# Kernel tuning notes

Measured on AMD Instinct MI355X. Metric: run time of the kernel, lower is better.

The kernel has to match this reference:

```python
import jax, jax.numpy as jnp
import numpy as np
import math

C, D, N = 10000, 128, 16384

def setup_inputs() -> dict:
    key = jax.random.key(0)
    kz, kmu = jax.random.split(key)
    z = jax.random.normal(kz, (N, D), dtype=jnp.float32)
    mu = jax.random.normal(kmu, (C, D), dtype=jnp.float32) * (6.0 / math.sqrt(2 * D))
    log_cov = jnp.zeros((1,), dtype=jnp.float32)
    prior_logits = jnp.zeros((C,), dtype=jnp.float32)
    return {"z": z, "mu": mu, "log_cov": log_cov, "prior_logits": prior_logits}

def reference(z, mu, log_cov, prior_logits):
    # m2[n,c] = ||z_n - mu_c||^2 = ||z_n||^2 - 2 z_n.mu_c + ||mu_c||^2 (GEMM form,
    # algebraically identical to the explicit broadcast-diff in the torch source)
    z_sq = jnp.sum(z * z, axis=-1, keepdims=True)          # [N,1]
    mu_sq = jnp.sum(mu * mu, axis=-1)                      # [C]
    cross = jnp.einsum('nd,cd->nc', z, mu)                 # [N,C] GEMM
    m2 = z_sq - 2.0 * cross + mu_sq[None, :]               # [N,C]
    lc = log_cov[0]
    var = jnp.exp(lc)
    log_det = D * lc
    log_prior = jax.nn.log_softmax(prior_logits, axis=0)   # [C]
    return log_prior[None, :] - 0.5 * (m2 / var + log_det)
```

## Files before the change

### kernel.cpp

```cpp
#include <hip/hip_runtime.h>

#define N_DIM 16384
#define C_DIM 10000
#define D_DIM 128
#define CT 79
#define C_PAD 10240
#define BM 64
#define BN 128
#define MT 256
#define ZPB 2048
#define MPB 1280

typedef __attribute__((ext_vector_type(8))) short bf16x8;
typedef __attribute__((ext_vector_type(4))) float f32x4;
typedef __attribute__((ext_vector_type(2))) unsigned int uint2v;

static __device__ __forceinline__ unsigned short f2bf(float x) {
  unsigned int u = __float_as_uint(x);
  u += 0x7fffu + ((u >> 16) & 1u);
  return (unsigned short)(u >> 16);
}

__global__ __launch_bounds__(256) void prep_kernel(
    const float* __restrict__ z, const float* __restrict__ mu,
    const float* __restrict__ log_cov, const float* __restrict__ prior,
    unsigned short* __restrict__ zb, unsigned short* __restrict__ mub,
    float* __restrict__ atbl, float* __restrict__ btbl, float* __restrict__ lse_out) {
  const int bid = blockIdx.x;
  const int tid = threadIdx.x;
  if (bid < ZPB + MPB) {
    const bool isz = bid < ZPB;
    const int lane = tid & 63;
    const int row = (isz ? bid : bid - ZPB) * 8 + ((tid >> 6) << 1) + (lane >> 5);
    const int col = (lane & 31) * 4;
    const int nrows = isz ? N_DIM : C_DIM;
    f32x4 v = {0.f, 0.f, 0.f, 0.f};
    if (row < nrows)
      v = *(const f32x4*)((isz ? z : mu) + (size_t)row * D_DIM + col);
    float ss = v[0]*v[0] + v[1]*v[1] + v[2]*v[2] + v[3]*v[3];
    #pragma unroll
    for (int off = 16; off; off >>= 1) ss += __shfl_down(ss, off, 32);
    float lc = log_cov[0];
    float iv = expf(-lc);
    if (isz) { v[0]*=iv; v[1]*=iv; v[2]*=iv; v[3]*=iv; }
    uint2v packed;
    packed[0] = (unsigned int)f2bf(v[0]) | ((unsigned int)f2bf(v[1]) << 16);
    packed[1] = (unsigned int)f2bf(v[2]) | ((unsigned int)f2bf(v[3]) << 16);
    int cb = (lane & 31) * 8;
    if (isz) {
      *(uint2v*)((char*)zb + (size_t)row * 256 + cb) = packed;
    } else {
      *(uint2v*)((char*)mub + (size_t)row * 256 + (cb ^ ((row & 7) << 4))) = packed;
    }
    if ((lane & 31) == 0) {
      if (isz) {
        atbl[row] = -0.5f * ss * iv;
      } else {
        btbl[row] = (row < C_DIM)
            ? (prior[row] - 0.5f * ss * iv - 0.5f * (float)D_DIM * lc) : 0.f;
      }
    }
  } else {
    __shared__ float red[256];
    const f32x4* p4 = (const f32x4*)prior;
    float m = -1e30f;
    for (int i = tid; i < C_DIM / 4; i += 256) {
      f32x4 v = p4[i];
      m = fmaxf(fmaxf(fmaxf(m, v[0]), fmaxf(v[1], v[2])), v[3]);
    }
    red[tid] = m; __syncthreads();
    for (int s = 128; s; s >>= 1) {
      if (tid < s) red[tid] = fmaxf(red[tid], red[tid + s]);
      __syncthreads();
    }
    float mx = red[0]; __syncthreads();
    float sum = 0.f;
    for (int i = tid; i < C_DIM / 4; i += 256) {
      f32x4 v = p4[i];
      sum += expf(v[0] - mx) + expf(v[1] - mx) + expf(v[2] - mx) + expf(v[3] - mx);
    }
    red[tid] = sum; __syncthreads();
    for (int s = 128; s; s >>= 1) {
      if (tid < s) red[tid] += red[tid + s];
      __syncthreads();
    }
    if (tid == 0) *lse_out = mx + logf(red[0]);
  }
}

__global__ __launch_bounds__(256, 4) void lda_main_kernel(
    const unsigned short* __restrict__ zb, const unsigned short* __restrict__ mub,
    const float* __restrict__ atbl, const float* __restrict__ btbl,
    const float* __restrict__ lse_p, const float* __restrict__ log_cov,
    float* __restrict__ out) {
  __shared__ char lds[BN * 256];

  const int ct = blockIdx.x;
  const int mt = blockIdx.y;
  const int tid = threadIdx.x;
  const int rbase = mt * BM;
  const int cbase = ct * BN;
  const int wid = tid >> 6;
  const int lane = tid & 63;
  const int l15 = lane & 15;
  const int lq = lane >> 4;

  {
    const char* gm = (const char*)mub + (size_t)cbase * 256 + wid * 8192 + lane * 16;
    char* lm = lds + wid * 8192;
    #pragma unroll
    for (int it = 0; it < 8; ++it)
      __builtin_amdgcn_global_load_lds(
          (const __attribute__((address_space(1))) void*)(gm + it * 1024),
          (__attribute__((address_space(3))) void*)(lm + it * 1024), 16, 0, 0);
  }

  const int zrow = rbase + wid * 16 + l15;
  bf16x8 zf[4];
  #pragma unroll
  for (int kk = 0; kk < 4; ++kk)
    zf[kk] = *(const bf16x8*)((const char*)zb + (size_t)zrow * 256 + kk * 64 + lq * 16);

  const int l31 = lane & 31;
  const float lse = lse_p[0];
  f32x4 btv = *(const f32x4*)&btbl[cbase + l31 * 4];
  btv[0] -= lse; btv[1] -= lse; btv[2] -= lse; btv[3] -= lse;

  __syncthreads();

  f32x4 acc[8] = {};
  #pragma unroll
  for (int kk = 0; kk < 4; ++kk) {
    const int kbyte = kk * 64 + lq * 16;
    bf16x8 mf[8];
    #pragma unroll
    for (int a = 0; a < 8; ++a) {
      int row = a * 16 + l15;
      mf[a] = *(const bf16x8*)(lds + row * 256 + (kbyte ^ ((row & 7) << 4)));
    }
    #pragma unroll
    for (int a = 0; a < 8; ++a)
      acc[a] = __builtin_amdgcn_mfma_f32_16x16x32_bf16(mf[a], zf[kk], acc[a], 0, 0, 0);
  }

  __syncthreads();

  const int mloc = wid * 16 + l15;
  #pragma unroll
  for (int a = 0; a < 8; ++a) {
    int cb4 = (a * 16 + lq * 4) * 4;
    *(f32x4*)(lds + mloc * 512 + (cb4 ^ ((mloc & 7) << 4))) = acc[a];
  }

  const int hl = lane >> 5;
  #pragma unroll
  for (int i = 0; i < 16; i += 2) {
    int m = wid * 16 + i + hl;
    int rowg = rbase + m;
    f32x4 t = *(const f32x4*)(lds + m * 512 + ((l31 * 16) ^ ((m & 7) << 4)));
    float av = atbl[rowg];
    int cg = cbase + l31 * 4;
    if (cg < C_DIM) {
      f32x4 v;
      #pragma unroll
      for (int r = 0; r < 4; ++r) v[r] = av + btv[r] + t[r];
      __builtin_nontemporal_store(v, (f32x4*)(out + (size_t)rowg * C_DIM + cg));
    }
  }
}

extern "C" void kernel_launch(void* const* d_in, const int* in_sizes, int n_in,
                              void* d_out, int out_size, void* d_ws, size_t ws_size,
                              hipStream_t stream) {
  const float* z     = (const float*)d_in[0];
  const float* mu    = (const float*)d_in[1];
  const float* lcov  = (const float*)d_in[2];
  const float* prior = (const float*)d_in[3];
  float* out = (float*)d_out;

  char* w = (char*)d_ws;
  unsigned short* zb  = (unsigned short*)w;
  unsigned short* mub = (unsigned short*)(w + 4194304);
  float* atbl = (float*)(w + 4194304 + 2621440);
  float* btbl = atbl + N_DIM;
  float* lse  = btbl + C_PAD;

  prep_kernel<<<ZPB + MPB + 1, 256, 0, stream>>>(z, mu, lcov, prior,
                                                 zb, mub, atbl, btbl, lse);
  dim3 grid(CT, MT);
  lda_main_kernel<<<grid, 256, 0, stream>>>(zb, mub, atbl, btbl, lse, lcov, out);
}
```

Baseline: 128.4 us.

## Load GEMM fragments directly from global per wave and drop shared mu staging

The main kernel no longer stages the mu tile into LDS with global_load_lds and no longer needs a block barrier before the MFMA loop. Each wave now owns a 32-column strip and reads mu and z fragments straight from global memory into registers, computing a 32x64 sub-tile. The epilogue transposes through a per-wave LDS region without barriers, and the prep kernel stops swizzling mu. Global and L2 traffic goes up because z fragments are re-read by all four waves, in exchange for removing the synchronization and the LDS loads.

After: 255.2 us. 1.99x slower.

```diff
diff --git a/kernel.cpp b/kernel.cpp
--- a/kernel.cpp
+++ b/kernel.cpp
@@ -47,11 +47,7 @@
     packed[0] = (unsigned int)f2bf(v[0]) | ((unsigned int)f2bf(v[1]) << 16);
     packed[1] = (unsigned int)f2bf(v[2]) | ((unsigned int)f2bf(v[3]) << 16);
     int cb = (lane & 31) * 8;
-    if (isz) {
-      *(uint2v*)((char*)zb + (size_t)row * 256 + cb) = packed;
-    } else {
-      *(uint2v*)((char*)mub + (size_t)row * 256 + (cb ^ ((row & 7) << 4))) = packed;
-    }
+    *(uint2v*)((char*)(isz ? zb : mub) + (size_t)row * 256 + cb) = packed;
     if ((lane & 31) == 0) {
       if (isz) {
         atbl[row] = -0.5f * ss * iv;
@@ -93,73 +89,62 @@
     const float* __restrict__ atbl, const float* __restrict__ btbl,
     const float* __restrict__ lse_p, const float* __restrict__ log_cov,
     float* __restrict__ out) {
-  __shared__ char lds[BN * 256];
+  __shared__ char lds[4 * 8192];
 
   const int ct = blockIdx.x;
   const int mt = blockIdx.y;
   const int tid = threadIdx.x;
-  const int rbase = mt * BM;
-  const int cbase = ct * BN;
   const int wid = tid >> 6;
   const int lane = tid & 63;
   const int l15 = lane & 15;
   const int lq = lane >> 4;
+  const int l7 = lane & 7;
+  const int rbase = mt * BM;
+  const int cwave = ct * BN + wid * 32;
 
-  {
-    const char* gm = (const char*)mub + (size_t)cbase * 256 + wid * 8192 + lane * 16;
-    char* lm = lds + wid * 8192;
+  const float lse = lse_p[0];
+  f32x4 btv = *(const f32x4*)&btbl[cwave + l7 * 4];
+  btv[0] -= lse; btv[1] -= lse; btv[2] -= lse; btv[3] -= lse;
+
+  f32x4 acc[2][4] = {};
+  #pragma unroll
+  for (int kk = 0; kk < 4; ++kk) {
+    const int kb = kk * 64 + lq * 16;
+    bf16x8 mf[2];
     #pragma unroll
-    for (int it = 0; it < 8; ++it)
-      __builtin_amdgcn_global_load_lds(
-          (const __attribute__((address_space(1))) void*)(gm + it * 1024),
-          (__attribute__((address_space(3))) void*)(lm + it * 1024), 16, 0, 0);
+    for (int cf = 0; cf < 2; ++cf)
+      mf[cf] = *(const bf16x8*)((const char*)mub +
+                 (size_t)(cwave + cf * 16 + l15) * 256 + kb);
+    bf16x8 zf[4];
+    #pragma unroll
+    for (int nf = 0; nf < 4; ++nf)
+      zf[nf] = *(const bf16x8*)((const char*)zb +
+                 (size_t)(rbase + nf * 16 + l15) * 256 + kb);
+    #pragma unroll
+    for (int cf = 0; cf < 2; ++cf)
+      #pragma unroll
+      for (int nf = 0; nf < 4; ++nf)
+        acc[cf][nf] = __builtin_amdgcn_mfma_f32_16x16x32_bf16(
+            mf[cf], zf[nf], acc[cf][nf], 0, 0, 0);
   }
 
-  const int zrow = rbase + wid * 16 + l15;
-  bf16x8 zf[4];
+  char* wlds = lds + wid * 8192;
   #pragma unroll
-  for (int kk = 0; kk < 4; ++kk)
-    zf[kk] = *(const bf16x8*)((const char*)zb + (size_t)zrow * 256 + kk * 64 + lq * 16);
+  for (int cf = 0; cf < 2; ++cf)
+    #pragma unroll
+    for (int nf = 0; nf < 4; ++nf) {
+      int m = nf * 16 + l15;
+      int cb4 = (cf * 16 + lq * 4) * 4;
+      *(f32x4*)(wlds + m * 128 + (cb4 ^ ((m & 7) << 4))) = acc[cf][nf];
+    }
 
-  const int l31 = lane & 31;
-  const float lse = lse_p[0];
-  f32x4 btv = *(const f32x4*)&btbl[cbase + l31 * 4];
-  btv[0] -= lse; btv[1] -= lse; btv[2] -= lse; btv[3] -= lse;
-
-  __syncthreads();
-
-  f32x4 acc[8] = {};
+  const int cg = cwave + l7 * 4;
   #pragma unroll
-  for (int kk = 0; kk < 4; ++kk) {
-    const int kbyte = kk * 64 + lq * 16;
-    bf16x8 mf[8];
-    #pragma unroll
-    for (int a = 0; a < 8; ++a) {
-      int row = a * 16 + l15;
-      mf[a] = *(const bf16x8*)(lds + row * 256 + (kbyte ^ ((row & 7) << 4)));
-    }
-    #pragma unroll
-    for (int a = 0; a < 8; ++a)
-      acc[a] = __builtin_amdgcn_mfma_f32_16x16x32_bf16(mf[a], zf[kk], acc[a], 0, 0, 0);
-  }
-
-  __syncthreads();
-
-  const int mloc = wid * 16 + l15;
-  #pragma unroll
-  for (int a = 0; a < 8; ++a) {
-    int cb4 = (a * 16 + lq * 4) * 4;
-    *(f32x4*)(lds + mloc * 512 + (cb4 ^ ((mloc & 7) << 4))) = acc[a];
-  }
-
-  const int hl = lane >> 5;
-  #pragma unroll
-  for (int i = 0; i < 16; i += 2) {
-    int m = wid * 16 + i + hl;
+  for (int i = 0; i < 8; ++i) {
+    int m = i * 8 + (lane >> 3);
     int rowg = rbase + m;
-    f32x4 t = *(const f32x4*)(lds + m * 512 + ((l31 * 16) ^ ((m & 7) << 4)));
+    f32x4 t = *(const f32x4*)(wlds + m * 128 + ((l7 * 16) ^ ((m & 7) << 4)));
     float av = atbl[rowg];
-    int cg = cbase + l31 * 4;
     if (cg < C_DIM) {
       f32x4 v;
       #pragma unroll
```
